# Performance work log

Hardware: AMD Instinct MI355X
Metric: run time of the kernel (lower is better)

Reference implementation:

```python
import jax, jax.numpy as jnp
import numpy as np

N_QUBITS = 4
N_LAYERS = 3
DIM = 2 ** N_QUBITS  # 16


def _apply_1q_const(state, U, w):
    # state: (B, 16) complex64; U: (2, 2) constant gate on wire w (wire 0 = most significant)
    B = state.shape[0]
    left, right = 2 ** w, 2 ** (N_QUBITS - w - 1)
    s = state.reshape(B, left, 2, right)
    s = jnp.einsum('ij,bajc->baic', U, s)
    return s.reshape(B, DIM)


def _apply_1q_batched(state, U, w):
    # U: (B, 2, 2) per-sample gate (data re-uploading RY angles)
    B = state.shape[0]
    left, right = 2 ** w, 2 ** (N_QUBITS - w - 1)
    s = state.reshape(B, left, 2, right)
    s = jnp.einsum('bij,bajc->baic', U, s)
    return s.reshape(B, DIM)


def _cnot(state, c, t):
    # flip target axis amplitudes where control == 1
    B = state.shape[0]
    s = state.reshape((B,) + (2,) * N_QUBITS)
    s = jnp.moveaxis(s, (1 + c, 1 + t), (N_QUBITS - 1, N_QUBITS))
    s = s.at[..., 1, :].set(s[..., 1, ::-1])
    s = jnp.moveaxis(s, (N_QUBITS - 1, N_QUBITS), (1 + c, 1 + t))
    return s.reshape(B, DIM)


def _ry_batched(theta):
    # (B,) -> (B, 2, 2) RY matrices (real, cast to complex)
    c, s = jnp.cos(theta / 2), jnp.sin(theta / 2)
    return jnp.stack([jnp.stack([c, -s], -1), jnp.stack([s, c], -1)], -2).astype(jnp.complex64)


def _rot(phi, theta, omega):
    # PennyLane Rot = RZ(omega) RY(theta) RZ(phi)
    c, s = jnp.cos(theta / 2), jnp.sin(theta / 2)
    row0 = jnp.stack([jnp.exp(-1j * (phi + omega) / 2) * c, -jnp.exp(1j * (phi - omega) / 2) * s])
    row1 = jnp.stack([jnp.exp(-1j * (phi - omega) / 2) * s, jnp.exp(1j * (phi + omega) / 2) * c])
    return jnp.stack([row0, row1]).astype(jnp.complex64)


def _circuit(angles, q_weights):
    # angles: (B, 4); q_weights: (3, 4, 3). Returns <Z_0> per sample, (B,)
    B = angles.shape[0]
    state = jnp.zeros((B, DIM), jnp.complex64).at[:, 0].set(1.0)
    for l in range(N_LAYERS):
        # AngleEmbedding(rotation='Y') — same inputs re-uploaded each layer
        for w in range(N_QUBITS):
            state = _apply_1q_batched(state, _ry_batched(angles[:, w]), w)
        # StronglyEntanglingLayers, single layer -> range r = 1
        for w in range(N_QUBITS):
            phi, theta, omega = q_weights[l, w, 0], q_weights[l, w, 1], q_weights[l, w, 2]
            state = _apply_1q_const(state, _rot(phi, theta, omega), w)
        for w in range(N_QUBITS):
            state = _cnot(state, w, (w + 1) % N_QUBITS)
    probs = jnp.abs(state.reshape(B, 2, DIM // 2)) ** 2
    return jnp.sum(probs[:, 0, :], -1) - jnp.sum(probs[:, 1, :], -1)


def setup_inputs() -> dict:
    key = jax.random.key(0)
    k0, k1, k2, k3 = jax.random.split(key, 4)
    N, H = 800000, 128
    edge_attr = jax.random.normal(k0, (N, H), dtype=jnp.float32)
    W_proj = jax.random.normal(k1, (N_QUBITS, H), dtype=jnp.float32) / np.sqrt(H)
    b_proj = jax.random.normal(k2, (N_QUBITS,), dtype=jnp.float32) * 0.01
    # TorchLayer default init: Uniform(0, 2*pi)
    q_weights = jax.random.uniform(k3, (N_LAYERS, N_QUBITS, 3), dtype=jnp.float32) * (2 * np.pi)
    return {"edge_attr": edge_attr, "W_proj": W_proj, "b_proj": b_proj, "q_weights": q_weights}


def reference(edge_attr, W_proj, b_proj, q_weights):
    q_in = jnp.tanh(edge_attr @ W_proj.T + b_proj) * jnp.pi  # (N, 4)
    z = _circuit(q_in, q_weights)                            # (N,)
    return jax.nn.sigmoid(z).reshape(-1, 1)
```

## Files before the change

### kernel.cpp

```cpp
#include <hip/hip_runtime.h>

#define NQ  4
#define DIM 16
#define NL  3
#define HD  128

__global__ __launch_bounds__(256) void rqa_kernel(
    const float* __restrict__ edge,
    const float* __restrict__ W,
    const float* __restrict__ b,
    const float* __restrict__ qw,
    float* __restrict__ out, int N)
{
    __shared__ float rotm[NL * NQ][4];
    __shared__ float4 part[256][5];

    const int tid = threadIdx.x;
    if (tid < NL * NQ) {
        float phi = qw[tid * 3 + 0];
        float th  = qw[tid * 3 + 1];
        float om  = qw[tid * 3 + 2];
        float ct, st, ca, sa, cb, sb;
        sincosf(0.5f * th, &st, &ct);
        sincosf(0.5f * (phi + om), &sa, &ca);
        sincosf(0.5f * (phi - om), &sb, &cb);
        rotm[tid][0] =  ca * ct;
        rotm[tid][1] = -sa * ct;
        rotm[tid][2] = -cb * st;
        rotm[tid][3] = -sb * st;
    }

    const int lane = tid & 63;
    const int wid  = tid >> 6;
    const int sub  = lane & 15;
    const int grp  = lane >> 4;

    const float4* __restrict__ Wv = (const float4*)W;
    const float4 w00 = Wv[0 * 32 + sub], w01 = Wv[0 * 32 + sub + 16];
    const float4 w10 = Wv[1 * 32 + sub], w11 = Wv[1 * 32 + sub + 16];
    const float4 w20 = Wv[2 * 32 + sub], w21 = Wv[2 * 32 + sub + 16];
    const float4 w30 = Wv[3 * 32 + sub], w31 = Wv[3 * 32 + sub + 16];

    const size_t blockRow0 = (size_t)blockIdx.x * 256;

    #pragma unroll 4
    for (int p = 0; p < 16; ++p) {
        const int local = wid * 64 + p * 4 + grp;
        const size_t r = blockRow0 + local;
        if (r < (size_t)N) {
            const float4* __restrict__ row = (const float4*)(edge + r * HD);
            const float4 x0 = row[sub];
            const float4 x1 = row[sub + 16];
            float a0 = x0.x*w00.x + x0.y*w00.y + x0.z*w00.z + x0.w*w00.w
                     + x1.x*w01.x + x1.y*w01.y + x1.z*w01.z + x1.w*w01.w;
            float a1 = x0.x*w10.x + x0.y*w10.y + x0.z*w10.z + x0.w*w10.w
                     + x1.x*w11.x + x1.y*w11.y + x1.z*w11.z + x1.w*w11.w;
            float a2 = x0.x*w20.x + x0.y*w20.y + x0.z*w20.z + x0.w*w20.w
                     + x1.x*w21.x + x1.y*w21.y + x1.z*w21.z + x1.w*w21.w;
            float a3 = x0.x*w30.x + x0.y*w30.y + x0.z*w30.z + x0.w*w30.w
                     + x1.x*w31.x + x1.y*w31.y + x1.z*w31.z + x1.w*w31.w;
            a0 += __shfl_xor(a0, 1); a0 += __shfl_xor(a0, 2);
            a1 += __shfl_xor(a1, 1); a1 += __shfl_xor(a1, 2);
            a2 += __shfl_xor(a2, 1); a2 += __shfl_xor(a2, 2);
            a3 += __shfl_xor(a3, 1); a3 += __shfl_xor(a3, 2);
            if ((sub & 3) == 0)
                part[local][sub >> 2] = make_float4(a0, a1, a2, a3);
        }
    }
    __syncthreads();

    const size_t gid = blockRow0 + tid;
    if (gid >= (size_t)N) return;

    const float4 p0 = part[tid][0];
    const float4 p1 = part[tid][1];
    const float4 p2 = part[tid][2];
    const float4 p3 = part[tid][3];
    float acc[NQ] = { p0.x + p1.x + p2.x + p3.x + b[0],
                      p0.y + p1.y + p2.y + p3.y + b[1],
                      p0.z + p1.z + p2.z + p3.z + b[2],
                      p0.w + p1.w + p2.w + p3.w + b[3] };

    const float PIF = 3.14159265358979323846f;
    float cy[NQ], sy[NQ];
    #pragma unroll
    for (int w = 0; w < NQ; ++w) {
        float a = PIF * tanhf(acc[w]);
        sincosf(0.5f * a, &sy[w], &cy[w]);
    }

    float sr[DIM], si[DIM];
    #pragma unroll
    for (int n = 0; n < DIM; ++n) { sr[n] = 0.f; si[n] = 0.f; }
    sr[0] = 1.f;

    for (int l = 0; l < NL; ++l) {
        #pragma unroll
        for (int w = 0; w < NQ; ++w) {
            const int str = 1 << (3 - w);
            const float c = cy[w], s = sy[w];
            #pragma unroll
            for (int i0 = 0; i0 < DIM; ++i0) {
                if (i0 & str) continue;
                const int i1 = i0 | str;
                float r0 = c * sr[i0] - s * sr[i1];
                float m0 = c * si[i0] - s * si[i1];
                float r1 = s * sr[i0] + c * sr[i1];
                float m1 = s * si[i0] + c * si[i1];
                sr[i0] = r0; si[i0] = m0; sr[i1] = r1; si[i1] = m1;
            }
        }
        #pragma unroll
        for (int w = 0; w < NQ; ++w) {
            const float ar = rotm[l * NQ + w][0];
            const float ai = rotm[l * NQ + w][1];
            const float br = rotm[l * NQ + w][2];
            const float bi = rotm[l * NQ + w][3];
            const int str = 1 << (3 - w);
            #pragma unroll
            for (int i0 = 0; i0 < DIM; ++i0) {
                if (i0 & str) continue;
                const int i1 = i0 | str;
                const float s0r = sr[i0], s0i = si[i0];
                const float s1r = sr[i1], s1i = si[i1];
                sr[i0] =  ar * s0r - ai * s0i + br * s1r - bi * s1i;
                si[i0] =  ar * s0i + ai * s0r + br * s1i + bi * s1r;
                sr[i1] = -br * s0r - bi * s0i + ar * s1r + ai * s1i;
                si[i1] = -br * s0i + bi * s0r + ar * s1i - ai * s1r;
            }
        }
        #pragma unroll
        for (int w = 0; w < NQ; ++w) {
            const int cb_ = 1 << (3 - w);
            const int tb_ = 1 << (3 - ((w + 1) & 3));
            #pragma unroll
            for (int n = 0; n < DIM; ++n) {
                if ((n & cb_) && !(n & tb_)) {
                    const int m = n | tb_;
                    float t0 = sr[n]; sr[n] = sr[m]; sr[m] = t0;
                    float t1 = si[n]; si[n] = si[m]; si[m] = t1;
                }
            }
        }
    }

    float z = 0.f;
    #pragma unroll
    for (int n = 0; n < DIM; ++n) {
        const float p = sr[n] * sr[n] + si[n] * si[n];
        z = (n < 8) ? (z + p) : (z - p);
    }
    out[gid] = 1.0f / (1.0f + expf(-z));
}

extern "C" void kernel_launch(void* const* d_in, const int* in_sizes, int n_in,
                              void* d_out, int out_size, void* d_ws, size_t ws_size,
                              hipStream_t stream) {
    const float* edge = (const float*)d_in[0];
    const float* W    = (const float*)d_in[1];
    const float* b    = (const float*)d_in[2];
    const float* qw   = (const float*)d_in[3];
    float* out = (float*)d_out;

    const int N = in_sizes[0] / HD;
    const int blocks = (N + 255) / 256;
    rqa_kernel<<<dim3(blocks), dim3(256), 0, stream>>>(edge, W, b, qw, out, N);
}
```

Before: 128.3 us.

## Split projection and circuit into two kernels with register prefetch and fused gates

Splits the fused kernel into a projection kernel that software-pipelines the row loads by prefetching the next row into registers, and a circuit kernel that reads the projected angles from the workspace. Each per-sample RY gate is merged with the following constant Rot gate on the same wire into one 2x2 complex gate, removing one gate application per wire per layer. The layer loop is fully unrolled. The split is meant to let the memory-bound projection run without the register pressure of the circuit code, at the cost of a second launch and a workspace round trip of 16 bytes per row.

```diff
diff --git a/kernel.cpp b/kernel.cpp
--- a/kernel.cpp
+++ b/kernel.cpp
@@ -1,19 +1,88 @@
 #include <hip/hip_runtime.h>
 
-#define NQ  4
-#define DIM 16
-#define NL  3
-#define HD  128
+#define NQ    4
+#define DIM   16
+#define NL    3
+#define HD    128
+#define NTHR  256
+#define PIF   3.14159265358979323846f
 
-__global__ __launch_bounds__(256) void rqa_kernel(
+__global__ __launch_bounds__(NTHR) void proj_kernel(
     const float* __restrict__ edge,
     const float* __restrict__ W,
     const float* __restrict__ b,
+    float4* __restrict__ ws,
+    int N)
+{
+    __shared__ float4 part[NTHR][5];
+
+    const int tid  = threadIdx.x;
+    const int lane = tid & 63;
+    const int wid  = tid >> 6;
+    const int sub  = lane & 15;
+    const int grp  = lane >> 4;
+
+    const float4* __restrict__ Wv = (const float4*)W;
+    const float4 w00 = Wv[0*32 + sub], w01 = Wv[0*32 + sub + 16];
+    const float4 w10 = Wv[1*32 + sub], w11 = Wv[1*32 + sub + 16];
+    const float4 w20 = Wv[2*32 + sub], w21 = Wv[2*32 + sub + 16];
+    const float4 w30 = Wv[3*32 + sub], w31 = Wv[3*32 + sub + 16];
+
+    const unsigned Nu = (unsigned)N;
+    const unsigned blockRow0 = blockIdx.x * NTHR;
+    const float4* __restrict__ ep = (const float4*)edge;
+
+    unsigned r0 = blockRow0 + wid * 64 + grp;
+    if (r0 >= Nu) r0 = Nu - 1;
+    float4 xa0 = ep[(size_t)r0 * 32 + sub];
+    float4 xa1 = ep[(size_t)r0 * 32 + sub + 16];
+
+    #pragma unroll
+    for (int p = 0; p < 16; ++p) {
+        float4 xb0, xb1;
+        if (p < 15) {
+            unsigned rn = blockRow0 + wid * 64 + (p + 1) * 4 + grp;
+            if (rn >= Nu) rn = Nu - 1;
+            xb0 = ep[(size_t)rn * 32 + sub];
+            xb1 = ep[(size_t)rn * 32 + sub + 16];
+        }
+        float a0 = xa0.x*w00.x + xa0.y*w00.y + xa0.z*w00.z + xa0.w*w00.w
+                 + xa1.x*w01.x + xa1.y*w01.y + xa1.z*w01.z + xa1.w*w01.w;
+        float a1 = xa0.x*w10.x + xa0.y*w10.y + xa0.z*w10.z + xa0.w*w10.w
+                 + xa1.x*w11.x + xa1.y*w11.y + xa1.z*w11.z + xa1.w*w11.w;
+        float a2 = xa0.x*w20.x + xa0.y*w20.y + xa0.z*w20.z + xa0.w*w20.w
+                 + xa1.x*w21.x + xa1.y*w21.y + xa1.z*w21.z + xa1.w*w21.w;
+        float a3 = xa0.x*w30.x + xa0.y*w30.y + xa0.z*w30.z + xa0.w*w30.w
+                 + xa1.x*w31.x + xa1.y*w31.y + xa1.z*w31.z + xa1.w*w31.w;
+        a0 += __shfl_xor(a0, 1); a0 += __shfl_xor(a0, 2);
+        a1 += __shfl_xor(a1, 1); a1 += __shfl_xor(a1, 2);
+        a2 += __shfl_xor(a2, 1); a2 += __shfl_xor(a2, 2);
+        a3 += __shfl_xor(a3, 1); a3 += __shfl_xor(a3, 2);
+        if ((sub & 3) == 0)
+            part[wid * 64 + p * 4 + grp][sub >> 2] = make_float4(a0, a1, a2, a3);
+        xa0 = xb0; xa1 = xb1;
+    }
+    __syncthreads();
+
+    const unsigned gid = blockRow0 + tid;
+    if (gid < Nu) {
+        const float4 p0 = part[tid][0];
+        const float4 p1 = part[tid][1];
+        const float4 p2 = part[tid][2];
+        const float4 p3 = part[tid][3];
+        ws[gid] = make_float4(p0.x + p1.x + p2.x + p3.x + b[0],
+                              p0.y + p1.y + p2.y + p3.y + b[1],
+                              p0.z + p1.z + p2.z + p3.z + b[2],
+                              p0.w + p1.w + p2.w + p3.w + b[3]);
+    }
+}
+
+__global__ __launch_bounds__(NTHR) void circ_kernel(
+    const float4* __restrict__ ws,
     const float* __restrict__ qw,
     float* __restrict__ out, int N)
 {
-    __shared__ float rotm[NL * NQ][4];
-    __shared__ float4 part[256][5];
+    __shared__ float4 rotm4[NL * NQ];
 
     const int tid = threadIdx.x;
     if (tid < NL * NQ) {
@@ -24,68 +93,20 @@
         sincosf(0.5f * th, &st, &ct);
         sincosf(0.5f * (phi + om), &sa, &ca);
         sincosf(0.5f * (phi - om), &sb, &cb);
-        rotm[tid][0] =  ca * ct;
-        rotm[tid][1] = -sa * ct;
-        rotm[tid][2] = -cb * st;
-        rotm[tid][3] = -sb * st;
-    }
-
-    const int lane = tid & 63;
-    const int wid  = tid >> 6;
-    const int sub  = lane & 15;
-    const int grp  = lane >> 4;
-
-    const float4* __restrict__ Wv = (const float4*)W;
-    const float4 w00 = Wv[0 * 32 + sub], w01 = Wv[0 * 32 + sub + 16];
-    const float4 w10 = Wv[1 * 32 + sub], w11 = Wv[1 * 32 + sub + 16];
-    const float4 w20 = Wv[2 * 32 + sub], w21 = Wv[2 * 32 + sub + 16];
-    const float4 w30 = Wv[3 * 32 + sub], w31 = Wv[3 * 32 + sub + 16];
-
-    const size_t blockRow0 = (size_t)blockIdx.x * 256;
-
-    #pragma unroll 4
-    for (int p = 0; p < 16; ++p) {
-        const int local = wid * 64 + p * 4 + grp;
-        const size_t r = blockRow0 + local;
-        if (r < (size_t)N) {
-            const float4* __restrict__ row = (const float4*)(edge + r * HD);
-            const float4 x0 = row[sub];
-            const float4 x1 = row[sub + 16];
-            float a0 = x0.x*w00.x + x0.y*w00.y + x0.z*w00.z + x0.w*w00.w
-                     + x1.x*w01.x + x1.y*w01.y + x1.z*w01.z + x1.w*w01.w;
-            float a1 = x0.x*w10.x + x0.y*w10.y + x0.z*w10.z + x0.w*w10.w
-                     + x1.x*w11.x + x1.y*w11.y + x1.z*w11.z + x1.w*w11.w;
-            float a2 = x0.x*w20.x + x0.y*w20.y + x0.z*w20.z + x0.w*w20.w
-                     + x1.x*w21.x + x1.y*w21.y + x1.z*w21.z + x1.w*w21.w;
-            float a3 = x0.x*w30.x + x0.y*w30.y + x0.z*w30.z + x0.w*w30.w
-                     + x1.x*w31.x + x1.y*w31.y + x1.z*w31.z + x1.w*w31.w;
-            a0 += __shfl_xor(a0, 1); a0 += __shfl_xor(a0, 2);
-            a1 += __shfl_xor(a1, 1); a1 += __shfl_xor(a1, 2);
-            a2 += __shfl_xor(a2, 1); a2 += __shfl_xor(a2, 2);
-            a3 += __shfl_xor(a3, 1); a3 += __shfl_xor(a3, 2);
-            if ((sub & 3) == 0)
-                part[local][sub >> 2] = make_float4(a0, a1, a2, a3);
-        }
+        rotm4[tid] = make_float4(ca * ct, -sa * ct, -cb * st, -sb * st);
     }
     __syncthreads();
 
-    const size_t gid = blockRow0 + tid;
-    if (gid >= (size_t)N) return;
+    const unsigned gid = blockIdx.x * NTHR + tid;
+    if (gid >= (unsigned)N) return;
 
-    const float4 p0 = part[tid][0];
-    const float4 p1 = part[tid][1];
-    const float4 p2 = part[tid][2];
-    const float4 p3 = part[tid][3];
-    float acc[NQ] = { p0.x + p1.x + p2.x + p3.x + b[0],
-                      p0.y + p1.y + p2.y + p3.y + b[1],
-                      p0.z + p1.z + p2.z + p3.z + b[2],
-                      p0.w + p1.w + p2.w + p3.w + b[3] };
+    const float4 accv = ws[gid];
+    const float accf[NQ] = {accv.x, accv.y, accv.z, accv.w};
 
-    const float PIF = 3.14159265358979323846f;
     float cy[NQ], sy[NQ];
     #pragma unroll
     for (int w = 0; w < NQ; ++w) {
-        float a = PIF * tanhf(acc[w]);
+        float a = PIF * tanhf(accf[w]);
         sincosf(0.5f * a, &sy[w], &cy[w]);
     }
 
@@ -94,39 +115,26 @@
     for (int n = 0; n < DIM; ++n) { sr[n] = 0.f; si[n] = 0.f; }
     sr[0] = 1.f;
 
+    #pragma unroll
     for (int l = 0; l < NL; ++l) {
         #pragma unroll
         for (int w = 0; w < NQ; ++w) {
-            const int str = 1 << (3 - w);
+            const float4 g = rotm4[l * 4 + w];
             const float c = cy[w], s = sy[w];
-            #pragma unroll
-            for (int i0 = 0; i0 < DIM; ++i0) {
-                if (i0 & str) continue;
-                const int i1 = i0 | str;
-                float r0 = c * sr[i0] - s * sr[i1];
-                float m0 = c * si[i0] - s * si[i1];
-                float r1 = s * sr[i0] + c * sr[i1];
-                float m1 = s * si[i0] + c * si[i1];
-                sr[i0] = r0; si[i0] = m0; sr[i1] = r1; si[i1] = m1;
-            }
-        }
-        #pragma unroll
-        for (int w = 0; w < NQ; ++w) {
-            const float ar = rotm[l * NQ + w][0];
-            const float ai = rotm[l * NQ + w][1];
-            const float br = rotm[l * NQ + w][2];
-            const float bi = rotm[l * NQ + w][3];
+            const float m0r = g.x * c + g.z * s;
+            const float m0i = g.y * c + g.w * s;
+            const float m1r = g.z * c - g.x * s;
+            const float m1i = g.w * c - g.y * s;
             const int str = 1 << (3 - w);
             #pragma unroll
             for (int i0 = 0; i0 < DIM; ++i0) {
                 if (i0 & str) continue;
                 const int i1 = i0 | str;
-                const float s0r = sr[i0], s0i = si[i0];
-                const float s1r = sr[i1], s1i = si[i1];
-                sr[i0] =  ar * s0r - ai * s0i + br * s1r - bi * s1i;
-                si[i0] =  ar * s0i + ai * s0r + br * s1i + bi * s1r;
-                sr[i1] = -br * s0r - bi * s0i + ar * s1r + ai * s1i;
-                si[i1] = -br * s0i + bi * s0r + ar * s1i - ai * s1r;
+                const float s0r = sr[i0], s0i = si[i0], s1r = sr[i1], s1i = si[i1];
+                sr[i0] =  m0r*s0r - m0i*s0i + m1r*s1r - m1i*s1i;
+                si[i0] =  m0r*s0i + m0i*s0r + m1r*s1i + m1i*s1r;
+                sr[i1] = -m1r*s0r - m1i*s0i + m0r*s1r + m0i*s1i;
+                si[i1] = -m1r*s0i + m1i*s0r + m0r*s1i - m0i*s1r;
             }
         }
         #pragma unroll
@@ -150,7 +158,7 @@
         const float p = sr[n] * sr[n] + si[n] * si[n];
         z = (n < 8) ? (z + p) : (z - p);
     }
-    out[gid] = 1.0f / (1.0f + expf(-z));
+    out[gid] = 1.f / (1.f + expf(-z));
 }
 
 extern "C" void kernel_launch(void* const* d_in, const int* in_sizes, int n_in,
@@ -160,9 +168,11 @@
     const float* W    = (const float*)d_in[1];
     const float* b    = (const float*)d_in[2];
     const float* qw   = (const float*)d_in[3];
-    float* out = (float*)d_out;
+    float* out  = (float*)d_out;
+    float4* ws  = (float4*)d_ws;
 
     const int N = in_sizes[0] / HD;
-    const int blocks = (N + 255) / 256;
-    rqa_kernel<<<dim3(blocks), dim3(256), 0, stream>>>(edge, W, b, qw, out, N);
+    const int blocks = (N + NTHR - 1) / NTHR;
+    proj_kernel<<<dim3(blocks), dim3(NTHR), 0, stream>>>(edge, W, b, ws, N);
+    circ_kernel<<<dim3(blocks), dim3(NTHR), 0, stream>>>(ws, qw, out, N);
 }
```

Measured after the change: 131.6 us. 2.5% more time.
